# Optimization experiments

Measured on AMD Instinct MI355X. Metric: run time of the kernel, lower is better.

Reference implementation:

```python
import jax, jax.numpy as jnp
import numpy as np
from jax.scipy.special import logsumexp

D = 1024      # d_model
H = 8         # num_heads
N = 16        # state_dim
ITERS = 5     # sinkhorn_iters
TAU = 1.0
B, S = 4, 1024
EPS = 1e-5


def setup_inputs() -> dict:
    key = jax.random.key(0)
    ks = jax.random.split(key, 8)
    x = jax.random.normal(ks[0], (B, S, D), dtype=jnp.float32)
    ln_w = jnp.ones((D,), jnp.float32)
    ln_b = jnp.zeros((D,), jnp.float32)
    # perm_proj: normal std=0.01, zero bias
    Wp = 0.01 * jax.random.normal(ks[1], (D, H * N * N), dtype=jnp.float32)
    bp = jnp.zeros((H * N * N,), jnp.float32)
    # gate_proj: normal std=0.01, bias=2.0
    Wg = 0.01 * jax.random.normal(ks[2], (D, H * N), dtype=jnp.float32)
    bg = jnp.full((H * N,), 2.0, jnp.float32)
    # input_proj / output_proj: xavier uniform, zero bias
    lim_i = float(np.sqrt(6.0 / (D + H * N)))
    Wi = jax.random.uniform(ks[3], (D, H * N), jnp.float32, -lim_i, lim_i)
    bi = jnp.zeros((H * N,), jnp.float32)
    Wo = jax.random.uniform(ks[4], (H * N, D), jnp.float32, -lim_i, lim_i)
    bo = jnp.zeros((D,), jnp.float32)
    return {"x": x, "ln_w": ln_w, "ln_b": ln_b, "Wp": Wp, "bp": bp,
            "Wg": Wg, "bg": bg, "Wi": Wi, "bi": bi, "Wo": Wo, "bo": bo}


def _sinkhorn(log_alpha):
    # log-space Sinkhorn: alternate row/column normalization
    for _ in range(ITERS):
        log_alpha = log_alpha - logsumexp(log_alpha, axis=-1, keepdims=True)
        log_alpha = log_alpha - logsumexp(log_alpha, axis=-2, keepdims=True)
    return jnp.exp(log_alpha)


def reference(x, ln_w, ln_b, Wp, bp, Wg, bg, Wi, bi, Wo, bo):
    residual = x
    # LayerNorm
    mu = jnp.mean(x, axis=-1, keepdims=True)
    var = jnp.var(x, axis=-1, keepdims=True)
    xn = (x - mu) * jax.lax.rsqrt(var + EPS) * ln_w + ln_b
    # projections
    logits = ((xn @ Wp + bp).reshape(B, S, H, N, N)) / TAU
    gamma = jax.nn.sigmoid((xn @ Wg + bg).reshape(B, S, H, N))
    b_in = (xn @ Wi + bi).reshape(B, S, H, N)
    # Sinkhorn for all timesteps at once (independent of recurrent state)
    soft = _sinkhorn(logits)                      # [B,S,H,N,N]
    # sequential state update over time
    Ps = jnp.moveaxis(soft, 1, 0)                 # [S,B,H,N,N]
    gs = jnp.moveaxis(gamma, 1, 0)                # [S,B,H,N]
    bs = jnp.moveaxis(b_in, 1, 0)                 # [S,B,H,N]

    def step(h, inp):
        P, g, b = inp
        h_perm = jnp.einsum('bhij,bhj->bhi', P, h)
        h_new = g * h_perm + (1.0 - g) * b
        return h_new, h_new

    h0 = jnp.zeros((B, H, N), x.dtype)
    _, hs = jax.lax.scan(step, h0, (Ps, gs, bs))  # hs: [S,B,H,N]
    out = jnp.moveaxis(hs, 0, 1).reshape(B, S, H * N)
    out = out @ Wo + bo                           # dropout = identity (eval)
    return residual + out
```

## Files before the change

kernel.cpp:

```cpp
#include <hip/hip_runtime.h>
#include <hip/hip_bf16.h>

#define D_    1024
#define H_    8
#define N_    16
#define B_    4
#define S_    1024
#define TOK   (B_*S_)
#define NPROJ 2304
#define CHUNK 32
#define NCHUNK (S_/CHUNK)
#define NCHAIN (B_*H_)

typedef __attribute__((ext_vector_type(8))) short bf16x8;
typedef __attribute__((ext_vector_type(4))) float f32x4;

typedef __attribute__((address_space(3))) void       as3_void;
typedef const __attribute__((address_space(1))) void as1_void;

__device__ __forceinline__ void gload_lds16(const void* g, void* l) {
    __builtin_amdgcn_global_load_lds((as1_void*)g, (as3_void*)l, 16, 0, 0);
}

__device__ __forceinline__ short f2bf(float f) {
    unsigned u = __builtin_bit_cast(unsigned, f);
    unsigned r = 0x7FFFu + ((u >> 16) & 1u);
    return (short)((u + r) >> 16);
}
__device__ __forceinline__ float bf2f(short s) {
    unsigned u = ((unsigned)(unsigned short)s) << 16;
    return __builtin_bit_cast(float, u);
}

template <int IMM>
__device__ __forceinline__ float swzf(float x) {
    return __builtin_bit_cast(float,
        __builtin_amdgcn_ds_swizzle(__builtin_bit_cast(int, x), IMM));
}
__device__ __forceinline__ float bpermf(int addr, float x) {
    return __builtin_bit_cast(float,
        __builtin_amdgcn_ds_bpermute(addr, __builtin_bit_cast(int, x)));
}
template <int CTRL>
__device__ __forceinline__ float dppmov(float x) {
    return __builtin_bit_cast(float,
        __builtin_amdgcn_update_dpp(0, __builtin_bit_cast(int, x),
                                    CTRL, 0xF, 0xF, true));
}
#define DPP_QX1  0xB1
#define DPP_QX2  0x4E
#define DPP_HMIR 0x141
#define DPP_ROR8 0x128

__global__ __launch_bounds__(256) void prep_kernel(const float* __restrict__ Wp,
                                                   const float* __restrict__ Wg,
                                                   const float* __restrict__ Wi,
                                                   const float* __restrict__ Wo,
                                                   short* __restrict__ WcatT,
                                                   short* __restrict__ WoT,
                                                   const float* __restrict__ x,
                                                   const float* __restrict__ lnw,
                                                   const float* __restrict__ lnb,
                                                   short* __restrict__ xn) {
    int id = blockIdx.x;
    if (id < 2432) {
        const float* src; short* dst; int srcW, Ksz, n_off, bx, by;
        if (id < 2048)      { src = Wp; dst = WcatT; srcW = 2048; Ksz = 1024; n_off = 0;
                              bx = id & 63;  by = id >> 6; }
        else if (id < 2176) { int q = id - 2048; src = Wg; dst = WcatT; srcW = 128; Ksz = 1024;
                              n_off = 2048; bx = q & 3; by = q >> 2; }
        else if (id < 2304) { int q = id - 2176; src = Wi; dst = WcatT; srcW = 128; Ksz = 1024;
                              n_off = 2176; bx = q & 3; by = q >> 2; }
        else                { int q = id - 2304; src = Wo; dst = WoT; srcW = 1024; Ksz = 128;
                              n_off = 0; bx = q & 31; by = q >> 5; }
        __shared__ float tile[32][33];
        int n0 = bx * 32, k0 = by * 32;
        int r  = threadIdx.x >> 3;
        int c4 = (threadIdx.x & 7) * 4;
        float4 v = *(const float4*)(src + (size_t)(k0 + r) * srcW + n0 + c4);
        tile[r][c4+0] = v.x; tile[r][c4+1] = v.y; tile[r][c4+2] = v.z; tile[r][c4+3] = v.w;
        __syncthreads();
        short4 o;
        o.x = f2bf(tile[c4+0][r]); o.y = f2bf(tile[c4+1][r]);
        o.z = f2bf(tile[c4+2][r]); o.w = f2bf(tile[c4+3][r]);
        *(short4*)(dst + (size_t)(n_off + n0 + r) * Ksz + k0 + c4) = o;
    } else {
        int row = id - 2432;
        int t = threadIdx.x;
        const float* xr = x + (size_t)row * D_;
        float4 v = *(const float4*)(xr + t * 4);
        float s  = v.x + v.y + v.z + v.w;
        float s2 = v.x*v.x + v.y*v.y + v.z*v.z + v.w*v.w;
        #pragma unroll
        for (int m = 1; m < 64; m <<= 1) { s += __shfl_xor(s, m); s2 += __shfl_xor(s2, m); }
        __shared__ float ps[4], ps2[4];
        if ((t & 63) == 0) { ps[t >> 6] = s; ps2[t >> 6] = s2; }
        __syncthreads();
        s  = ps[0] + ps[1] + ps[2] + ps[3];
        s2 = ps2[0] + ps2[1] + ps2[2] + ps2[3];
        float mu  = s * (1.0f / D_);
        float var = s2 * (1.0f / D_) - mu * mu;
        float inv = rsqrtf(var + 1e-5f);
        float4 wv = *(const float4*)(lnw + t * 4);
        float4 bv = *(const float4*)(lnb + t * 4);
        short4 o;
        o.x = f2bf((v.x - mu) * inv * wv.x + bv.x);
        o.y = f2bf((v.y - mu) * inv * wv.y + bv.y);
        o.z = f2bf((v.z - mu) * inv * wv.z + bv.z);
        o.w = f2bf((v.w - mu) * inv * wv.w + bv.w);
        *(short4*)(xn + (size_t)row * D_ + t * 4) = o;
    }
}

template <int MODE>
__global__ __launch_bounds__(512) void gemm_bt(const short* __restrict__ A,
                                               const short* __restrict__ BT,
                                               void* __restrict__ Cout,
                                               int M, int N, int K,
                                               const float* __restrict__ bias0,
                                               const float* __restrict__ bias1,
                                               const float* __restrict__ bias2,
                                               const float* __restrict__ resid) {
    __shared__ short lA[2][128 * 32];
    __shared__ short lB[2][128 * 32];
    const int nwg = gridDim.x;
    const int cpx = nwg >> 3;
    const int orig = blockIdx.x;
    const int wg = (orig & 7) * cpx + (orig >> 3);
    const int ntn = N >> 7;
    const int m0 = (wg / ntn) * 128, n0 = (wg % ntn) * 128;
    const int t = threadIdx.x, w = t >> 6, l = t & 63;
    const int wm = w >> 2, wn = w & 3;
    const int sr = l >> 2;
    const int sg = (l & 3) ^ ((l >> 3) & 3);
    const int fr = l & 15, fg = l >> 4;
    const int frag_off = fr * 32 + 8 * (fg ^ ((fr >> 1) & 3));

    f32x4 acc[4][2];
    #pragma unroll
    for (int mi = 0; mi < 4; ++mi)
        #pragma unroll
        for (int ni = 0; ni < 2; ++ni) acc[mi][ni] = (f32x4){0.f, 0.f, 0.f, 0.f};

    auto STAGE = [&](int bi, int k0) {
        int row = w * 16 + sr;
        gload_lds16(A  + (size_t)(m0 + row) * K + k0 + sg * 8, &lA[bi][w * 512]);
        gload_lds16(BT + (size_t)(n0 + row) * K + k0 + sg * 8, &lB[bi][w * 512]);
    };

    const int NT = K >> 5;
    STAGE(0, 0);
    if (NT > 1) STAGE(1, 32);
    asm volatile("s_waitcnt vmcnt(2)" ::: "memory");
    __builtin_amdgcn_s_barrier();

    int cur = 0;
    for (int kt = 0; kt < NT; ++kt) {
        bf16x8 af[4], bfr[2];
        #pragma unroll
        for (int mi = 0; mi < 4; ++mi)
            af[mi] = *(const bf16x8*)(&lA[cur][(wm * 4 + mi) * 512] + frag_off);
        #pragma unroll
        for (int ni = 0; ni < 2; ++ni)
            bfr[ni] = *(const bf16x8*)(&lB[cur][(wn * 2 + ni) * 512] + frag_off);
        asm volatile("s_waitcnt lgkmcnt(0)" ::: "memory");
        __builtin_amdgcn_sched_barrier(0);
        __builtin_amdgcn_s_barrier();
        if (kt + 2 < NT) STAGE(cur, (kt + 2) << 5);
        __builtin_amdgcn_s_setprio(1);
        #pragma unroll
        for (int mi = 0; mi < 4; ++mi)
            #pragma unroll
            for (int ni = 0; ni < 2; ++ni)
                acc[mi][ni] = __builtin_amdgcn_mfma_f32_16x16x32_bf16(af[mi], bfr[ni], acc[mi][ni], 0, 0, 0);
        __builtin_amdgcn_s_setprio(0);
        if (kt + 1 < NT) {
            if (kt + 2 < NT) asm volatile("s_waitcnt vmcnt(2)" ::: "memory");
            else             asm volatile("s_waitcnt vmcnt(0)" ::: "memory");
            __builtin_amdgcn_sched_barrier(0);
            __builtin_amdgcn_s_barrier();
        }
        cur ^= 1;
    }

    const int cr = (l >> 4) * 4, cc = l & 15;
    #pragma unroll
    for (int mi = 0; mi < 4; ++mi)
        #pragma unroll
        for (int ni = 0; ni < 2; ++ni) {
            int col = n0 + wn * 32 + ni * 16 + cc;
            float badd;
            if (MODE == 0)
                badd = (col < 2048) ? bias0[col] : (col < 2176 ? bias1[col - 2048] : bias2[col - 2176]);
            else
                badd = bias0[col];
            #pragma unroll
            for (int e = 0; e < 4; ++e) {
                int row = m0 + wm * 64 + mi * 16 + cr + e;
                float vout = acc[mi][ni][e] + badd;
                if (MODE == 0) {
                    ((short*)Cout)[(size_t)row * N + col] = f2bf(vout);
                } else {
                    vout += resid[(size_t)row * N + col];
                    ((float*)Cout)[(size_t)row * N + col] = vout;
                }
            }
        }
}

__global__ __launch_bounds__(256) void sinkhorn_kernel(const short* __restrict__ Cp,
                                                       short* __restrict__ Ahat,
                                                       float* __restrict__ u) {
    int w = threadIdx.x >> 6, l = threadIdx.x & 63;
    int id = blockIdx.x * 4 + w;
    int r = id >> 3, hh = id & 7;
    int a = l >> 3, b = l & 7;
    const short* base = Cp + (size_t)r * NPROJ + hh * 256;
    short2 q0 = *(const short2*)(base + (2 * a)     * 16 + 2 * b);
    short2 q1 = *(const short2*)(base + (2 * a + 1) * 16 + 2 * b);
    float p00 = __expf(bf2f(q0.x)), p01 = __expf(bf2f(q0.y));
    float p10 = __expf(bf2f(q1.x)), p11 = __expf(bf2f(q1.y));
    const int a32 = ((l ^ 32) << 2);
    #pragma unroll
    for (int it = 0; it < 5; ++it) {
        float r0 = p00 + p01, r1 = p10 + p11;
        r0 += dppmov<DPP_QX1>(r0);  r1 += dppmov<DPP_QX1>(r1);
        r0 += dppmov<DPP_QX2>(r0);  r1 += dppmov<DPP_QX2>(r1);
        r0 += dppmov<DPP_HMIR>(r0); r1 += dppmov<DPP_HMIR>(r1);
        float i0 = __builtin_amdgcn_rcpf(r0), i1 = __builtin_amdgcn_rcpf(r1);
        p00 *= i0; p01 *= i0; p10 *= i1; p11 *= i1;
        float c0 = p00 + p10, c1 = p01 + p11;
        c0 += dppmov<DPP_ROR8>(c0); c1 += dppmov<DPP_ROR8>(c1);
        c0 += swzf<0x401F>(c0);     c1 += swzf<0x401F>(c1);
        c0 += bpermf(a32, c0);      c1 += bpermf(a32, c1);
        float j0 = __builtin_amdgcn_rcpf(c0), j1 = __builtin_amdgcn_rcpf(c1);
        p00 *= j0; p10 *= j0; p01 *= j1; p11 *= j1;
    }
    short2 gp = *(const short2*)(Cp + (size_t)r * NPROJ + 2048 + hh * 16 + 2 * a);
    short2 bn = *(const short2*)(Cp + (size_t)r * NPROJ + 2176 + hh * 16 + 2 * a);
    float g0 = 1.f / (1.f + __expf(-bf2f(gp.x)));
    float g1 = 1.f / (1.f + __expf(-bf2f(gp.y)));
    short2 o0, o1;
    o0.x = f2bf(g0 * p00); o0.y = f2bf(g0 * p01);
    o1.x = f2bf(g1 * p10); o1.y = f2bf(g1 * p11);
    short* Ao = Ahat + (size_t)id * 256;
    *(short2*)(Ao + (2 * a)     * 16 + 2 * b) = o0;
    *(short2*)(Ao + (2 * a + 1) * 16 + 2 * b) = o1;
    if (b == 0) {
        float2 uo;
        uo.x = (1.f - g0) * bf2f(bn.x);
        uo.y = (1.f - g1) * bf2f(bn.y);
        *(float2*)(u + (size_t)id * 16 + 2 * a) = uo;
    }
}

__global__ __launch_bounds__(64) void pass1_kernel(const short* __restrict__ Ahat,
                                                   const float* __restrict__ u,
                                                   short* __restrict__ Mc,
                                                   float* __restrict__ vc) {
    __shared__ short lAh[CHUNK * 256];
    __shared__ float lu[CHUNK * 16];
    int unit = blockIdx.x;
    int chain = unit >> 5, c = unit & 31;
    int b = chain >> 3, hh = chain & 7;
    int l = threadIdx.x;
    int j = l & 15, g = l >> 4;
    const size_t id0 = ((size_t)(b * S_ + c * CHUNK)) * H_ + hh;

    #pragma unroll
    for (int q = 0; q < 16; ++q) {
        int m = q * 2 + (l >> 5);
        gload_lds16(Ahat + (id0 + (size_t)m * H_) * 256 + (l & 31) * 8,
                    (char*)lAh + q * 1024);
    }
    #pragma unroll
    for (int q = 0; q < 2; ++q) {
        int sl = q * 16 + (l >> 2);
        gload_lds16(u + (id0 + (size_t)sl * H_) * 16 + (l & 3) * 4,
                    (char*)lu + q * 1024);
    }
    asm volatile("s_waitcnt vmcnt(0)" ::: "memory");

    bf16x8 mb = {0,0,0,0,0,0,0,0};
    bf16x8 vb = {0,0,0,0,0,0,0,0};
    #pragma unroll
    for (int e = 0; e < 4; ++e) if (4 * g + e == j) mb[e] = (short)0x3F80;
    const f32x4 zero = {0.f, 0.f, 0.f, 0.f};
    f32x4 d = zero, dv = zero;
    #pragma unroll 4
    for (int tt = 0; tt < CHUNK; ++tt) {
        short4 pa = *(const short4*)(&lAh[tt * 256 + j * 16 + g * 4]);
        bf16x8 af = {0,0,0,0,0,0,0,0};
        af[0] = pa.x; af[1] = pa.y; af[2] = pa.z; af[3] = pa.w;
        d  = __builtin_amdgcn_mfma_f32_16x16x32_bf16(af, mb, zero, 0, 0, 0);
        dv = __builtin_amdgcn_mfma_f32_16x16x32_bf16(af, vb, zero, 0, 0, 0);
        if (j == 0) {
            dv[0] += lu[tt * 16 + 4 * g + 0];
            dv[1] += lu[tt * 16 + 4 * g + 1];
            dv[2] += lu[tt * 16 + 4 * g + 2];
            dv[3] += lu[tt * 16 + 4 * g + 3];
        }
        mb[0] = f2bf(d[0]);  mb[1] = f2bf(d[1]);  mb[2] = f2bf(d[2]);  mb[3] = f2bf(d[3]);
        vb[0] = f2bf(dv[0]); vb[1] = f2bf(dv[1]); vb[2] = f2bf(dv[2]); vb[3] = f2bf(dv[3]);
    }
    short* Mo = Mc + (size_t)unit * 256;
    #pragma unroll
    for (int e = 0; e < 4; ++e) Mo[(4 * g + e) * 16 + j] = mb[e];
    if (j == 0) {
        #pragma unroll
        for (int e = 0; e < 4; ++e) vc[(size_t)unit * 16 + 4 * g + e] = dv[e];
    }
}

__global__ __launch_bounds__(64) void pass23_kernel(const short* __restrict__ Ahat,
                                                    const float* __restrict__ u,
                                                    const short* __restrict__ Mc,
                                                    const float* __restrict__ vc,
                                                    short* __restrict__ hs) {
    __shared__ short mats[64 * 256];
    __shared__ float vecs[64 * 16];
    int unit = blockIdx.x;
    int chain = unit >> 5, c = unit & 31;
    int b = chain >> 3, hh = chain & 7;
    int l = threadIdx.x, i = l & 15, g = l >> 4;
    const size_t id0 = ((size_t)(b * S_ + c * CHUNK)) * H_ + hh;

    #pragma unroll
    for (int q = 0; q < 16; ++q) {
        int m = q * 2 + (l >> 5);
        gload_lds16(Ahat + (id0 + (size_t)m * H_) * 256 + (l & 31) * 8,
                    (char*)mats + q * 1024);
    }
    #pragma unroll
    for (int q = 0; q < 2; ++q) {
        int sl = q * 16 + (l >> 2);
        gload_lds16(u + (id0 + (size_t)sl * H_) * 16 + (l & 3) * 4,
                    (char*)vecs + q * 1024);
    }
    const short* McB = Mc + (size_t)chain * NCHUNK * 256;
    const int nmc = (c + 1) >> 1;
    for (int q = 0; q < nmc; ++q)
        gload_lds16(McB + q * 512 + l * 8, (char*)mats + 16384 + q * 1024);
    const float* vcB = vc + (size_t)chain * NCHUNK * 16;
    const int nvc = (c + 15) >> 4;
    for (int q = 0; q < nvc; ++q)
        gload_lds16(vcB + q * 256 + l * 4, (char*)vecs + 2048 + q * 1024);

    asm volatile("s_waitcnt vmcnt(0)" ::: "memory");

    float h_0 = 0.f, h_1 = 0.f, h_2 = 0.f, h_3 = 0.f;
    for (int cc = 0; cc < c; ++cc) {
        short4 pa = *(const short4*)(&mats[(32 + cc) * 256 + i * 16 + g * 4]);
        float part = bf2f(pa.x) * h_0 + bf2f(pa.y) * h_1 + bf2f(pa.z) * h_2 + bf2f(pa.w) * h_3;
        part += __shfl_xor(part, 16);
        part += __shfl_xor(part, 32);
        float hnew = part + vecs[(32 + cc) * 16 + i];
        h_0 = __shfl(hnew, 4 * g + 0);
        h_1 = __shfl(hnew, 4 * g + 1);
        h_2 = __shfl(hnew, 4 * g + 2);
        h_3 = __shfl(hnew, 4 * g + 3);
    }
    #pragma unroll 4
    for (int tt = 0; tt < CHUNK; ++tt) {
        size_t r = (size_t)b * S_ + c * CHUNK + tt;
        short4 pa = *(const short4*)(&mats[tt * 256 + i * 16 + g * 4]);
        float part = bf2f(pa.x) * h_0 + bf2f(pa.y) * h_1 + bf2f(pa.z) * h_2 + bf2f(pa.w) * h_3;
        part += __shfl_xor(part, 16);
        part += __shfl_xor(part, 32);
        float hnew = part + vecs[tt * 16 + i];
        if (g == 0) hs[r * 128 + hh * 16 + i] = f2bf(hnew);
        h_0 = __shfl(hnew, 4 * g + 0);
        h_1 = __shfl(hnew, 4 * g + 1);
        h_2 = __shfl(hnew, 4 * g + 2);
        h_3 = __shfl(hnew, 4 * g + 3);
    }
}

extern "C" void kernel_launch(void* const* d_in, const int* in_sizes, int n_in,
                              void* d_out, int out_size, void* d_ws, size_t ws_size,
                              hipStream_t stream) {
    const float* x    = (const float*)d_in[0];
    const float* ln_w = (const float*)d_in[1];
    const float* ln_b = (const float*)d_in[2];
    const float* Wp   = (const float*)d_in[3];
    const float* bp   = (const float*)d_in[4];
    const float* Wg   = (const float*)d_in[5];
    const float* bg   = (const float*)d_in[6];
    const float* Wi   = (const float*)d_in[7];
    const float* bi   = (const float*)d_in[8];
    const float* Wo   = (const float*)d_in[9];
    const float* bo   = (const float*)d_in[10];
    float* out = (float*)d_out;

    char* ws = (char*)d_ws;
    constexpr size_t OFF_WCATT = 0;
    constexpr size_t OFF_WOT   = OFF_WCATT + (size_t)NPROJ * D_ * 2;
    constexpr size_t OFF_XN    = OFF_WOT   + (size_t)D_ * 128 * 2;
    constexpr size_t OFF_CP    = OFF_XN    + (size_t)TOK * D_ * 2;
    constexpr size_t OFF_AHAT  = OFF_CP    + (size_t)TOK * NPROJ * 2;
    constexpr size_t OFF_U     = OFF_AHAT  + (size_t)TOK * H_ * 256 * 2;
    constexpr size_t OFF_MC    = OFF_U     + (size_t)TOK * H_ * 16 * 4;
    constexpr size_t OFF_VC    = OFF_MC    + (size_t)NCHAIN * NCHUNK * 256 * 2;
    constexpr size_t OFF_HS    = OFF_VC    + (size_t)NCHAIN * NCHUNK * 16 * 4;

    short* WcatT = (short*)(ws + OFF_WCATT);
    short* WoT   = (short*)(ws + OFF_WOT);
    short* xn    = (short*)(ws + OFF_XN);
    short* Cp    = (short*)(ws + OFF_CP);
    short* Ahat  = (short*)(ws + OFF_AHAT);
    float* u     = (float*)(ws + OFF_U);
    short* Mc    = (short*)(ws + OFF_MC);
    float* vc    = (float*)(ws + OFF_VC);
    short* hs    = (short*)(ws + OFF_HS);

    prep_kernel<<<2432 + TOK, 256, 0, stream>>>(Wp, Wg, Wi, Wo, WcatT, WoT,
                                                x, ln_w, ln_b, xn);
    gemm_bt<0><<<(NPROJ / 128) * (TOK / 128), 512, 0, stream>>>(
        xn, WcatT, (void*)Cp, TOK, NPROJ, 1024, bp, bg, bi, nullptr);
    sinkhorn_kernel<<<(TOK * H_) / 4, 256, 0, stream>>>(Cp, Ahat, u);
    pass1_kernel<<<NCHAIN * NCHUNK, 64, 0, stream>>>(Ahat, u, Mc, vc);
    pass23_kernel<<<NCHAIN * NCHUNK, 64, 0, stream>>>(Ahat, u, Mc, vc, hs);
    gemm_bt<1><<<(D_ / 128) * (TOK / 128), 512, 0, stream>>>(
        hs, WoT, (void*)out, TOK, D_, 128, bo, nullptr, nullptr, x);
}
```

Before: 92.22 us.

## Fuse Sinkhorn normalization into chunk-scan pass1 kernel via LDS staging

Merges the per-token Sinkhorn kernel with the first chunked-scan pass. Each 256-thread block runs Sinkhorn for the 32 tokens of one chunk, writes the gated matrices and bias vectors straight into LDS, and then one wave runs the MFMA chunk composition. This removes one kernel launch and the global re-read of Ahat and u in pass1. In exchange, only 1024 blocks now do the Sinkhorn work with an 8-step serial loop per wave, and three waves sit idle during the serial scan, which may reduce parallelism and latency hiding.

```diff
diff --git a/kernel.cpp b/kernel.cpp
--- a/kernel.cpp
+++ b/kernel.cpp
@@ -208,107 +208,97 @@
         }
 }
 
-__global__ __launch_bounds__(256) void sinkhorn_kernel(const short* __restrict__ Cp,
-                                                       short* __restrict__ Ahat,
-                                                       float* __restrict__ u) {
-    int w = threadIdx.x >> 6, l = threadIdx.x & 63;
-    int id = blockIdx.x * 4 + w;
-    int r = id >> 3, hh = id & 7;
-    int a = l >> 3, b = l & 7;
-    const short* base = Cp + (size_t)r * NPROJ + hh * 256;
-    short2 q0 = *(const short2*)(base + (2 * a)     * 16 + 2 * b);
-    short2 q1 = *(const short2*)(base + (2 * a + 1) * 16 + 2 * b);
-    float p00 = __expf(bf2f(q0.x)), p01 = __expf(bf2f(q0.y));
-    float p10 = __expf(bf2f(q1.x)), p11 = __expf(bf2f(q1.y));
-    const int a32 = ((l ^ 32) << 2);
-    #pragma unroll
-    for (int it = 0; it < 5; ++it) {
-        float r0 = p00 + p01, r1 = p10 + p11;
-        r0 += dppmov<DPP_QX1>(r0);  r1 += dppmov<DPP_QX1>(r1);
-        r0 += dppmov<DPP_QX2>(r0);  r1 += dppmov<DPP_QX2>(r1);
-        r0 += dppmov<DPP_HMIR>(r0); r1 += dppmov<DPP_HMIR>(r1);
-        float i0 = __builtin_amdgcn_rcpf(r0), i1 = __builtin_amdgcn_rcpf(r1);
-        p00 *= i0; p01 *= i0; p10 *= i1; p11 *= i1;
-        float c0 = p00 + p10, c1 = p01 + p11;
-        c0 += dppmov<DPP_ROR8>(c0); c1 += dppmov<DPP_ROR8>(c1);
-        c0 += swzf<0x401F>(c0);     c1 += swzf<0x401F>(c1);
-        c0 += bpermf(a32, c0);      c1 += bpermf(a32, c1);
-        float j0 = __builtin_amdgcn_rcpf(c0), j1 = __builtin_amdgcn_rcpf(c1);
-        p00 *= j0; p10 *= j0; p01 *= j1; p11 *= j1;
-    }
-    short2 gp = *(const short2*)(Cp + (size_t)r * NPROJ + 2048 + hh * 16 + 2 * a);
-    short2 bn = *(const short2*)(Cp + (size_t)r * NPROJ + 2176 + hh * 16 + 2 * a);
-    float g0 = 1.f / (1.f + __expf(-bf2f(gp.x)));
-    float g1 = 1.f / (1.f + __expf(-bf2f(gp.y)));
-    short2 o0, o1;
-    o0.x = f2bf(g0 * p00); o0.y = f2bf(g0 * p01);
-    o1.x = f2bf(g1 * p10); o1.y = f2bf(g1 * p11);
-    short* Ao = Ahat + (size_t)id * 256;
-    *(short2*)(Ao + (2 * a)     * 16 + 2 * b) = o0;
-    *(short2*)(Ao + (2 * a + 1) * 16 + 2 * b) = o1;
-    if (b == 0) {
-        float2 uo;
-        uo.x = (1.f - g0) * bf2f(bn.x);
-        uo.y = (1.f - g1) * bf2f(bn.y);
-        *(float2*)(u + (size_t)id * 16 + 2 * a) = uo;
-    }
-}
-
-__global__ __launch_bounds__(64) void pass1_kernel(const short* __restrict__ Ahat,
-                                                   const float* __restrict__ u,
-                                                   short* __restrict__ Mc,
-                                                   float* __restrict__ vc) {
+__global__ __launch_bounds__(256) void sinkpass1_kernel(const short* __restrict__ Cp,
+                                                        short* __restrict__ Ahat,
+                                                        float* __restrict__ u_g,
+                                                        short* __restrict__ Mc,
+                                                        float* __restrict__ vc) {
     __shared__ short lAh[CHUNK * 256];
     __shared__ float lu[CHUNK * 16];
-    int unit = blockIdx.x;
-    int chain = unit >> 5, c = unit & 31;
-    int b = chain >> 3, hh = chain & 7;
-    int l = threadIdx.x;
-    int j = l & 15, g = l >> 4;
-    const size_t id0 = ((size_t)(b * S_ + c * CHUNK)) * H_ + hh;
-
-    #pragma unroll
-    for (int q = 0; q < 16; ++q) {
-        int m = q * 2 + (l >> 5);
-        gload_lds16(Ahat + (id0 + (size_t)m * H_) * 256 + (l & 31) * 8,
-                    (char*)lAh + q * 1024);
-    }
-    #pragma unroll
-    for (int q = 0; q < 2; ++q) {
-        int sl = q * 16 + (l >> 2);
-        gload_lds16(u + (id0 + (size_t)sl * H_) * 16 + (l & 3) * 4,
-                    (char*)lu + q * 1024);
-    }
-    asm volatile("s_waitcnt vmcnt(0)" ::: "memory");
-
-    bf16x8 mb = {0,0,0,0,0,0,0,0};
-    bf16x8 vb = {0,0,0,0,0,0,0,0};
-    #pragma unroll
-    for (int e = 0; e < 4; ++e) if (4 * g + e == j) mb[e] = (short)0x3F80;
-    const f32x4 zero = {0.f, 0.f, 0.f, 0.f};
-    f32x4 d = zero, dv = zero;
-    #pragma unroll 4
-    for (int tt = 0; tt < CHUNK; ++tt) {
-        short4 pa = *(const short4*)(&lAh[tt * 256 + j * 16 + g * 4]);
-        bf16x8 af = {0,0,0,0,0,0,0,0};
-        af[0] = pa.x; af[1] = pa.y; af[2] = pa.z; af[3] = pa.w;
-        d  = __builtin_amdgcn_mfma_f32_16x16x32_bf16(af, mb, zero, 0, 0, 0);
-        dv = __builtin_amdgcn_mfma_f32_16x16x32_bf16(af, vb, zero, 0, 0, 0);
+    const int unit = blockIdx.x;
+    const int chain = unit >> 5, c = unit & 31;
+    const int b = chain >> 3, hh = chain & 7;
+    const int tid = threadIdx.x, w = tid >> 6, l = tid & 63;
+    const int a = l >> 3, bl = l & 7;
+    const int a32 = ((l ^ 32) << 2);
+
+    for (int k = 0; k < 8; ++k) {
+        const int tt = w * 8 + k;
+        const int tok = b * S_ + c * CHUNK + tt;
+        const short* base = Cp + (size_t)tok * NPROJ + hh * 256;
+        short2 q0 = *(const short2*)(base + (2 * a)     * 16 + 2 * bl);
+        short2 q1 = *(const short2*)(base + (2 * a + 1) * 16 + 2 * bl);
+        float p00 = __expf(bf2f(q0.x)), p01 = __expf(bf2f(q0.y));
+        float p10 = __expf(bf2f(q1.x)), p11 = __expf(bf2f(q1.y));
+        #pragma unroll
+        for (int it = 0; it < 5; ++it) {
+            float r0 = p00 + p01, r1 = p10 + p11;
+            r0 += dppmov<DPP_QX1>(r0);  r1 += dppmov<DPP_QX1>(r1);
+            r0 += dppmov<DPP_QX2>(r0);  r1 += dppmov<DPP_QX2>(r1);
+            r0 += dppmov<DPP_HMIR>(r0); r1 += dppmov<DPP_HMIR>(r1);
+            float i0 = __builtin_amdgcn_rcpf(r0), i1 = __builtin_amdgcn_rcpf(r1);
+            p00 *= i0; p01 *= i0; p10 *= i1; p11 *= i1;
+            float c0 = p00 + p10, c1 = p01 + p11;
+            c0 += dppmov<DPP_ROR8>(c0); c1 += dppmov<DPP_ROR8>(c1);
+            c0 += swzf<0x401F>(c0);     c1 += swzf<0x401F>(c1);
+            c0 += bpermf(a32, c0);      c1 += bpermf(a32, c1);
+            float j0 = __builtin_amdgcn_rcpf(c0), j1 = __builtin_amdgcn_rcpf(c1);
+            p00 *= j0; p10 *= j0; p01 *= j1; p11 *= j1;
+        }
+        short2 gp = *(const short2*)(Cp + (size_t)tok * NPROJ + 2048 + hh * 16 + 2 * a);
+        short2 bn = *(const short2*)(Cp + (size_t)tok * NPROJ + 2176 + hh * 16 + 2 * a);
+        float g0 = 1.f / (1.f + __expf(-bf2f(gp.x)));
+        float g1 = 1.f / (1.f + __expf(-bf2f(gp.y)));
+        short2 o0, o1;
+        o0.x = f2bf(g0 * p00); o0.y = f2bf(g0 * p01);
+        o1.x = f2bf(g1 * p10); o1.y = f2bf(g1 * p11);
+        short* Al = lAh + tt * 256;
+        *(short2*)(Al + (2 * a)     * 16 + 2 * bl) = o0;
+        *(short2*)(Al + (2 * a + 1) * 16 + 2 * bl) = o1;
+        short* Ag = Ahat + ((size_t)tok * H_ + hh) * 256;
+        *(short2*)(Ag + (2 * a)     * 16 + 2 * bl) = o0;
+        *(short2*)(Ag + (2 * a + 1) * 16 + 2 * bl) = o1;
+        if (bl == 0) {
+            float2 uu;
+            uu.x = (1.f - g0) * bf2f(bn.x);
+            uu.y = (1.f - g1) * bf2f(bn.y);
+            *(float2*)(&lu[tt * 16 + 2 * a]) = uu;
+            *(float2*)(u_g + ((size_t)tok * H_ + hh) * 16 + 2 * a) = uu;
+        }
+    }
+    __syncthreads();
+
+    if (w == 0) {
+        const int j = l & 15, g = l >> 4;
+        bf16x8 mb = {0,0,0,0,0,0,0,0};
+        bf16x8 vb = {0,0,0,0,0,0,0,0};
+        #pragma unroll
+        for (int e = 0; e < 4; ++e) if (4 * g + e == j) mb[e] = (short)0x3F80;
+        const f32x4 zero = {0.f, 0.f, 0.f, 0.f};
+        f32x4 d = zero, dv = zero;
+        #pragma unroll 4
+        for (int tt = 0; tt < CHUNK; ++tt) {
+            short4 pa = *(const short4*)(&lAh[tt * 256 + j * 16 + g * 4]);
+            bf16x8 af = {0,0,0,0,0,0,0,0};
+            af[0] = pa.x; af[1] = pa.y; af[2] = pa.z; af[3] = pa.w;
+            d  = __builtin_amdgcn_mfma_f32_16x16x32_bf16(af, mb, zero, 0, 0, 0);
+            dv = __builtin_amdgcn_mfma_f32_16x16x32_bf16(af, vb, zero, 0, 0, 0);
+            if (j == 0) {
+                dv[0] += lu[tt * 16 + 4 * g + 0];
+                dv[1] += lu[tt * 16 + 4 * g + 1];
+                dv[2] += lu[tt * 16 + 4 * g + 2];
+                dv[3] += lu[tt * 16 + 4 * g + 3];
+            }
+            mb[0] = f2bf(d[0]);  mb[1] = f2bf(d[1]);  mb[2] = f2bf(d[2]);  mb[3] = f2bf(d[3]);
+            vb[0] = f2bf(dv[0]); vb[1] = f2bf(dv[1]); vb[2] = f2bf(dv[2]); vb[3] = f2bf(dv[3]);
+        }
+        short* Mo = Mc + (size_t)unit * 256;
+        #pragma unroll
+        for (int e = 0; e < 4; ++e) Mo[(4 * g + e) * 16 + j] = mb[e];
         if (j == 0) {
-            dv[0] += lu[tt * 16 + 4 * g + 0];
-            dv[1] += lu[tt * 16 + 4 * g + 1];
-            dv[2] += lu[tt * 16 + 4 * g + 2];
-            dv[3] += lu[tt * 16 + 4 * g + 3];
-        }
-        mb[0] = f2bf(d[0]);  mb[1] = f2bf(d[1]);  mb[2] = f2bf(d[2]);  mb[3] = f2bf(d[3]);
-        vb[0] = f2bf(dv[0]); vb[1] = f2bf(dv[1]); vb[2] = f2bf(dv[2]); vb[3] = f2bf(dv[3]);
-    }
-    short* Mo = Mc + (size_t)unit * 256;
-    #pragma unroll
-    for (int e = 0; e < 4; ++e) Mo[(4 * g + e) * 16 + j] = mb[e];
-    if (j == 0) {
-        #pragma unroll
-        for (int e = 0; e < 4; ++e) vc[(size_t)unit * 16 + 4 * g + e] = dv[e];
+            #pragma unroll
+            for (int e = 0; e < 4; ++e) vc[(size_t)unit * 16 + 4 * g + e] = dv[e];
+        }
     }
 }
 
@@ -417,8 +407,7 @@
                                                 x, ln_w, ln_b, xn);
     gemm_bt<0><<<(NPROJ / 128) * (TOK / 128), 512, 0, stream>>>(
         xn, WcatT, (void*)Cp, TOK, NPROJ, 1024, bp, bg, bi, nullptr);
-    sinkhorn_kernel<<<(TOK * H_) / 4, 256, 0, stream>>>(Cp, Ahat, u);
-    pass1_kernel<<<NCHAIN * NCHUNK, 64, 0, stream>>>(Ahat, u, Mc, vc);
+    sinkpass1_kernel<<<NCHAIN * NCHUNK, 256, 0, stream>>>(Cp, Ahat, u, Mc, vc);
     pass23_kernel<<<NCHAIN * NCHUNK, 64, 0, stream>>>(Ahat, u, Mc, vc, hs);
     gemm_bt<1><<<(D_ / 128) * (TOK / 128), 512, 0, stream>>>(
         hs, WoT, (void*)out, TOK, D_, 128, bo, nullptr, nullptr, x);
```

Result: no change. 91.69 us, median of 2 (-0.6%).
